# Performance work log

Hardware: AMD Instinct MI355X
Metric: run time of the kernel (lower is better)

Reference implementation:

```python
import jax, jax.numpy as jnp
import numpy as np

B, L, H, V = 64, 8, 4096, 50257


def setup_inputs() -> dict:
    key = jax.random.key(0)
    ks = jax.random.split(key, 5)
    return {
        "embedding": jax.random.normal(ks[0], (V, H), jnp.float32) * 0.02,
        "hidden_states": jax.random.normal(ks[1], (B, L, H), jnp.float32),
        "output_position": 7,  # scalar index of the position to sample from
        "temperatures": jax.random.uniform(ks[2], (B,), jnp.float32, 0.5, 1.5),
        "top_ps": jax.random.uniform(ks[3], (B,), jnp.float32, 0.7, 1.0),
        "tops_ks": jax.random.randint(ks[4], (B,), 1, 64),  # top-k in [1,64)
        "embedding_bias": jnp.zeros((V,), jnp.float32),
    }


def reference(embedding, hidden_states, output_position, temperatures, top_ps, tops_ks, embedding_bias):
    # select the output position: [B, H]
    h = hidden_states[:, output_position, :]
    # logits GEMM against tied embedding: [B, V]
    logits = jnp.einsum("bh,vh->bv", h, embedding) + embedding_bias[None, :]
    logits = logits / temperatures[:, None]
    probs = jax.nn.softmax(logits.astype(jnp.float32), axis=-1)

    # descending sort of probabilities
    order = jnp.argsort(-probs, axis=-1)                       # [B, V]
    probs_sort = jnp.take_along_axis(probs, order, axis=-1)    # [B, V]

    # top-p mask: exclusive cumulative sum exceeding top_p
    cum = jnp.cumsum(probs_sort, axis=-1)
    topp_mask = (cum - probs_sort) > top_ps[:, None]
    # top-k mask: rank >= k
    ranks = jnp.arange(V, dtype=tops_ks.dtype)[None, :]
    topk_mask = ranks >= tops_ks[:, None]

    probs_sort = jnp.where(topp_mask | topk_mask, 0.0, probs_sort)
    probs_sort = probs_sort / jnp.sum(probs_sort, axis=-1, keepdims=True)

    # scatter back to original vocab order via inverse permutation
    inv = jnp.argsort(order, axis=-1)
    probs_final = jnp.take_along_axis(probs_sort, inv, axis=-1)  # [B, V]

    # multinomial sampling (1 sample per row)
    logp = jnp.where(probs_final > 0, jnp.log(jnp.maximum(probs_final, 1e-38)), -jnp.inf)
    next_token_ids = jax.random.categorical(jax.random.key(42), logp, axis=-1)
    return next_token_ids
```

## Files before the change

### kernel.cpp

```cpp
#include <hip/hip_runtime.h>
#include <stdint.h>
#include <float.h>
#include <limits.h>


typedef __bf16 bf16x8 __attribute__((ext_vector_type(8)));
typedef float  f32x4  __attribute__((ext_vector_type(4)));

__device__ __forceinline__ void split8v(const float* f, bf16x8& hi, bf16x8& lo) {
#pragma unroll
    for (int e = 0; e < 8; ++e) {
        const __bf16 h = (__bf16)f[e];
        hi[e] = h;
        lo[e] = (__bf16)(f[e] - (float)h);
    }
}
__device__ __forceinline__ void split8(const float* f, uint4& hi, uint4& lo) {
    bf16x8 vh, vl;
    split8v(f, vh, vl);
    hi = __builtin_bit_cast(uint4, vh);
    lo = __builtin_bit_cast(uint4, vl);
}

__global__ __launch_bounds__(256) void prep_h(
    const float* __restrict__ hs, const int* __restrict__ pos_p,
    unsigned short* __restrict__ Ahi, unsigned short* __restrict__ Alo,
    int H, int L)
{
    const int pos = pos_p[0];
    const int tid = blockIdx.x * 256 + threadIdx.x;
    const int b     = tid >> 8;
    const int kbase = (tid & 255) * 16;
    const float* src = hs + ((size_t)b * L + pos) * H + kbase;
    float f[16];
    *(float4*)&f[0]  = *(const float4*)(src);
    *(float4*)&f[4]  = *(const float4*)(src + 4);
    *(float4*)&f[8]  = *(const float4*)(src + 8);
    *(float4*)&f[12] = *(const float4*)(src + 12);

    const int r16 = b >> 4, ll = b & 15;
    const int kc  = kbase >> 5;
    const int lh0 = (kbase >> 3) & 3;
#pragma unroll
    for (int c = 0; c < 2; ++c) {
        uint4 hi, lo;
        split8(f + 8 * c, hi, lo);
        const size_t dst = ((size_t)(r16 * (H >> 5) + kc) * 64 + (lh0 + c) * 16 + ll) * 8;
        *(uint4*)&Ahi[dst] = hi;
        *(uint4*)&Alo[dst] = lo;
    }
}

#define NWF    512
#define WTILES 16

__global__ __launch_bounds__(256, 2) void logits_mfma(
    const float* __restrict__ emb,
    const unsigned short* __restrict__ Ahi,
    const unsigned short* __restrict__ Alo,
    const float* __restrict__ temps,
    const float* __restrict__ bias,
    float*       __restrict__ out,
    int V, int H)
{
    __shared__ float sB[2][16 * NWF];

    const int tid  = threadIdx.x;
    const int lane = tid & 63;
    const int w    = tid >> 6;
    const int v0   = blockIdx.x * 16;

    const int ll = lane & 15;
    const int lh = lane >> 4;

    const int NWIN = H / NWF;
    const int NTT  = H >> 5;
    const int wst  = (blockIdx.x & 3) * 2;

    const size_t aoff = (size_t)w * ((size_t)H * 16)
                      + (size_t)lh * 128 + (size_t)ll * 8;

    bf16x8 aih[2], ail[2];
    f32x4  acc = (f32x4){0.f, 0.f, 0.f, 0.f};

#define STAGE(win, bf) do {                                                   \
    _Pragma("unroll")                                                         \
    for (int rr = 0; rr < 4; ++rr) {                                          \
        const int r = w * 4 + rr;                                             \
        int rg = v0 + r;                                                      \
        rg = (rg < V) ? rg : (V - 1);                                         \
        const float* rowp = emb + (size_t)rg * H + (size_t)(win) * NWF        \
                          + ((lane * 4) ^ ((r & 15) << 2));                   \
        _Pragma("unroll")                                                     \
        for (int c = 0; c < 2; ++c) {                                         \
            __builtin_amdgcn_global_load_lds(                                 \
                (const __attribute__((address_space(1))) void*)(rowp + c * 256), \
                (__attribute__((address_space(3))) void*)&sB[bf][r * NWF + c * 256], \
                16, 0, 0);                                                    \
        }                                                                     \
    }                                                                         \
} while (0)

#define LOADA(T, p) do {                                                      \
    const size_t ai = aoff + (size_t)(T) * 512;                               \
    aih[p] = *(const bf16x8*)&Ahi[ai];                                        \
    ail[p] = *(const bf16x8*)&Alo[ai];                                        \
} while (0)

    LOADA(wst * WTILES, 0);
    STAGE(wst, 0);
    __syncthreads();

    for (int ws = 0; ws < NWIN; ++ws) {
        const int bf = ws & 1;
        if (ws + 1 < NWIN) STAGE((wst + ws + 1) & (NWIN - 1), bf ^ 1);

#pragma unroll
        for (int kt = 0; kt < WTILES; ++kt) {
            const int p = kt & 1;
            if (!(ws == NWIN - 1 && kt == WTILES - 1)) {
                const int wsn = ws + ((kt + 1) >> 4);
                const int ktn = (kt + 1) & 15;
                const int T1  = (((wst + wsn) & (NWIN - 1)) << 4) + ktn;
                LOADA(T1, p ^ 1);
            }

            const int f0   = kt * 32 + lh * 8;
            const int sidx = ll << 2;
            float f[8];
            *(float4*)&f[0] = *(const float4*)&sB[bf][ll * NWF + ((f0)     ^ sidx)];
            *(float4*)&f[4] = *(const float4*)&sB[bf][ll * NWF + ((f0 + 4) ^ sidx)];
            bf16x8 fbh, fbl;
            split8v(f, fbh, fbl);

            acc = __builtin_amdgcn_mfma_f32_16x16x32_bf16(ail[p], fbh, acc, 0, 0, 0);
            acc = __builtin_amdgcn_mfma_f32_16x16x32_bf16(aih[p], fbl, acc, 0, 0, 0);
            acc = __builtin_amdgcn_mfma_f32_16x16x32_bf16(aih[p], fbh, acc, 0, 0, 0);
        }
        __syncthreads();
    }
#undef STAGE
#undef LOADA

    const int vv = v0 + ll;
    if (vv < V) {
        const float bv = bias[vv];
#pragma unroll
        for (int r = 0; r < 4; ++r) {
            const int b = w * 16 + lh * 4 + r;
            out[(size_t)b * V + vv] = (acc[r] + bv) / temps[b];
        }
    }
}

__device__ __forceinline__ uint32_t rotl32(uint32_t x, int d) {
    return (x << d) | (x >> (32 - d));
}

__device__ float jax_gumbel(uint32_t flat) {
    const uint32_t k0 = 0u, k1 = 42u;
    const uint32_t ks[3] = { k0, k1, k0 ^ k1 ^ 0x1BD11BDAu };
    uint32_t x0 = 0u   + ks[0];
    uint32_t x1 = flat + ks[1];
    const int rot[2][4] = { {13, 15, 26, 6}, {17, 29, 16, 24} };
#pragma unroll
    for (int r = 0; r < 5; ++r) {
        const int* rr = rot[r & 1];
#pragma unroll
        for (int j = 0; j < 4; ++j) {
            x0 += x1;
            x1 = rotl32(x1, rr[j]);
            x1 ^= x0;
        }
        x0 += ks[(r + 1) % 3];
        x1 += ks[(r + 2) % 3] + (uint32_t)(r + 1);
    }
    const uint32_t bits = x0 ^ x1;
    const uint32_t fb = (bits >> 9) | 0x3F800000u;
    const float f = __uint_as_float(fb) - 1.0f;
    const float tiny = 1.17549435e-38f;
    float u = __fadd_rn(__fmul_rn(f, 1.0f), tiny);
    u = fmaxf(tiny, u);
    const float l1 = logf(u);
    return -logf(-l1);
}

#define NBINS 4096
#define CAP   2048
#define NKEEP 64

__global__ __launch_bounds__(256) void sample_kernel(
    const float* __restrict__ logits,
    const float* __restrict__ top_ps,
    const int*   __restrict__ top_ks,
    int*         __restrict__ out_ids,
    int V)
{
    const int b = blockIdx.x;
    const int tid = threadIdx.x;
    const float* row = logits + (size_t)b * V;

    __shared__ float swred[4];
    __shared__ int   bins[NBINS];
    __shared__ int   schunk[256];
    __shared__ int   sThrBin, sCnt, sMkeep;
    __shared__ float cval[CAP];
    __shared__ int   cidx[CAP];
    __shared__ float tval[NKEEP];
    __shared__ int   tidxs[NKEEP];

    float m = -INFINITY;
    for (int k = tid; k < V; k += 256) m = fmaxf(m, row[k]);
#pragma unroll
    for (int o = 32; o > 0; o >>= 1) m = fmaxf(m, __shfl_xor(m, o, 64));
    if ((tid & 63) == 0) swred[tid >> 6] = m;
    __syncthreads();
    m = fmaxf(fmaxf(swred[0], swred[1]), fmaxf(swred[2], swred[3]));

    for (int k = tid; k < NBINS; k += 256) bins[k] = 0;
    if (tid == 0) sCnt = 0;
    __syncthreads();

    float s = 0.f;
    for (int k = tid; k < V; k += 256) {
        const float x = row[k];
        s += expf(x - m);
        const float g = m - x;
        int bin = (int)(g * 256.0f);
        if (bin >= NBINS) bin = NBINS - 1;
        atomicAdd(&bins[bin], 1);
    }
#pragma unroll
    for (int o = 32; o > 0; o >>= 1) s += __shfl_xor(s, o, 64);
    __syncthreads();
    if ((tid & 63) == 0) swred[tid >> 6] = s;

    int csum = 0;
#pragma unroll
    for (int k = 0; k < NBINS / 256; ++k) csum += bins[tid * (NBINS / 256) + k];
    schunk[tid] = csum;
    __syncthreads();
    s = swred[0] + swred[1] + swred[2] + swred[3];
    if (tid == 0) {
        int cum = 0, chunk = 255;
        for (int c = 0; c < 256; ++c) {
            if (cum + schunk[c] >= NKEEP) { chunk = c; break; }
            cum += schunk[c];
        }
        int t = NBINS - 1;
        const int base = chunk * (NBINS / 256);
        for (int k = base; k < base + NBINS / 256; ++k) {
            cum += bins[k];
            if (cum >= NKEEP) { t = k; break; }
        }
        sThrBin = t;
    }
    __syncthreads();
    const int thrBin = sThrBin;

    for (int k = tid; k < V; k += 256) {
        const float x = row[k];
        const float g = m - x;
        int bin = (int)(g * 256.0f);
        if (bin >= NBINS) bin = NBINS - 1;
        if (bin <= thrBin) {
            const int p = atomicAdd(&sCnt, 1);
            if (p < CAP) { cval[p] = x; cidx[p] = k; }
        }
    }
    __syncthreads();
    const int C = min(sCnt, CAP);

    for (int i = tid; i < C; i += 256) {
        const float vi = cval[i];
        const int   ii = cidx[i];
        int rank = 0;
        for (int j = 0; j < C; ++j) {
            const float vj = cval[j];
            const int   ij = cidx[j];
            rank += (vj > vi) || (vj == vi && ij < ii);
        }
        if (rank < NKEEP) { tval[rank] = vi; tidxs[rank] = ii; }
    }
    __syncthreads();

    if (tid == 0) {
        const float pb = top_ps[b];
        const int   kk = top_ks[b];
        const int   nk = min(NKEEP, C);
        float cum = 0.f;
        int mk = 0;
        for (int r = 0; r < nk; ++r) {
            const float pr = expf(tval[r] - m) / s;
            cum += pr;
            const float excl = cum - pr;
            if (excl > pb || r >= kk) break;
            ++mk;
        }
        sMkeep = (mk > 0) ? mk : 1;
    }
    __syncthreads();
    const int mkeep = sMkeep;

    if (tid < 64) {
        float sc = -INFINITY;
        int vid = INT_MAX;
        if (tid < mkeep) {
            const int v = tidxs[tid];
            vid = v;
            sc = tval[tid] + jax_gumbel((uint32_t)b * (uint32_t)V + (uint32_t)v);
        }
#pragma unroll
        for (int o = 32; o > 0; o >>= 1) {
            const float os = __shfl_xor(sc, o, 64);
            const int   ov = __shfl_xor(vid, o, 64);
            if (os > sc || (os == sc && ov < vid)) { sc = os; vid = ov; }
        }
        if (tid == 0) out_ids[b] = vid;
    }
}

extern "C" void kernel_launch(void* const* d_in, const int* in_sizes, int n_in,
                              void* d_out, int out_size, void* d_ws, size_t ws_size,
                              hipStream_t stream)
{
    const float* emb   = (const float*)d_in[0];
    const float* hs    = (const float*)d_in[1];
    const int*   pos   = (const int*)d_in[2];
    const float* temps = (const float*)d_in[3];
    const float* tps   = (const float*)d_in[4];
    const int*   tks   = (const int*)d_in[5];
    const float* bias  = (const float*)d_in[6];

    const int B = in_sizes[3];
    const int V = in_sizes[6];
    const int H = (int)((long long)in_sizes[0] / V);
    const int L = (int)((long long)in_sizes[1] / ((long long)B * H));

    float*          logits = (float*)d_ws;
    unsigned short* Ahi    = (unsigned short*)((char*)d_ws + (16u << 20));
    unsigned short* Alo    = Ahi + (size_t)B * H;

    prep_h<<<(B * H) / (16 * 256), 256, 0, stream>>>(hs, pos, Ahi, Alo, H, L);

    const int nblk = (V + 15) / 16;
    logits_mfma<<<nblk, 256, 0, stream>>>(emb, Ahi, Alo, temps, bias,
                                          logits, V, H);

    sample_kernel<<<B, 256, 0, stream>>>(logits, tps, tks, (int*)d_out, V);
}
```

Measured before the change: 381.7 us.

## Replace double-buffered K windows with a 4-slot LDS ring and explicit vmcnt waits

Restructures the logits MFMA main loop to use smaller 256-wide K windows staged into a 4-deep LDS ring, with A fragments for a whole window loaded into registers in ping-pong sets. Synchronisation uses manual s_waitcnt vmcnt counts plus s_barrier instead of __syncthreads, and sched_barrier pins the instruction order, so two windows of loads stay in flight while one is computed. The per-block staggered starting window is removed. The hand-counted vmcnt values and the extra register pressure from 32 A vectors carry correctness and occupancy risks. With no barrier after each compute, ring slots could in principle be overwritten while still being read.

New measurement: 390.4 us. +2.3%, slower.

```diff
diff --git a/kernel.cpp b/kernel.cpp
--- a/kernel.cpp
+++ b/kernel.cpp
@@ -51,8 +51,8 @@
     }
 }
 
-#define NWF    512
-#define WTILES 16
+#define NWF 256
+#define RING 4
 
 __global__ __launch_bounds__(256, 2) void logits_mfma(
     const float* __restrict__ emb,
@@ -63,84 +63,103 @@
     float*       __restrict__ out,
     int V, int H)
 {
-    __shared__ float sB[2][16 * NWF];
+    __shared__ float sB[RING][16 * NWF];
 
     const int tid  = threadIdx.x;
     const int lane = tid & 63;
     const int w    = tid >> 6;
     const int v0   = blockIdx.x * 16;
 
-    const int ll = lane & 15;
-    const int lh = lane >> 4;
-
-    const int NWIN = H / NWF;
-    const int NTT  = H >> 5;
-    const int wst  = (blockIdx.x & 3) * 2;
+    const int ll  = lane & 15;
+    const int lh  = lane >> 4;
+    const int swz = ll << 2;
+
+    const int NW = H / NWF;
 
     const size_t aoff = (size_t)w * ((size_t)H * 16)
                       + (size_t)lh * 128 + (size_t)ll * 8;
 
-    bf16x8 aih[2], ail[2];
+    bf16x8 Ah0[8], Al0[8], Ah1[8], Al1[8];
     f32x4  acc = (f32x4){0.f, 0.f, 0.f, 0.f};
 
-#define STAGE(win, bf) do {                                                   \
+#define LOADA(win, AH, AL) do {                                               \
+    _Pragma("unroll")                                                         \
+    for (int kt = 0; kt < 8; ++kt) {                                          \
+        const size_t ai = aoff + ((size_t)(win) * 8 + kt) * 512;              \
+        AH[kt] = *(const bf16x8*)&Ahi[ai];                                    \
+        AL[kt] = *(const bf16x8*)&Alo[ai];                                    \
+    }                                                                         \
+} while (0)
+
+#define STAGE(win, slot) do {                                                 \
     _Pragma("unroll")                                                         \
     for (int rr = 0; rr < 4; ++rr) {                                          \
         const int r = w * 4 + rr;                                             \
         int rg = v0 + r;                                                      \
         rg = (rg < V) ? rg : (V - 1);                                         \
-        const float* rowp = emb + (size_t)rg * H + (size_t)(win) * NWF        \
+        const float* srcp = emb + (size_t)rg * H + (size_t)(win) * NWF        \
                           + ((lane * 4) ^ ((r & 15) << 2));                   \
-        _Pragma("unroll")                                                     \
-        for (int c = 0; c < 2; ++c) {                                         \
-            __builtin_amdgcn_global_load_lds(                                 \
-                (const __attribute__((address_space(1))) void*)(rowp + c * 256), \
-                (__attribute__((address_space(3))) void*)&sB[bf][r * NWF + c * 256], \
-                16, 0, 0);                                                    \
-        }                                                                     \
+        __builtin_amdgcn_global_load_lds(                                     \
+            (const __attribute__((address_space(1))) void*)srcp,              \
+            (__attribute__((address_space(3))) void*)&sB[slot][r * NWF],      \
+            16, 0, 0);                                                        \
     }                                                                         \
 } while (0)
 
-#define LOADA(T, p) do {                                                      \
-    const size_t ai = aoff + (size_t)(T) * 512;                               \
-    aih[p] = *(const bf16x8*)&Ahi[ai];                                        \
-    ail[p] = *(const bf16x8*)&Alo[ai];                                        \
+#define COMPUTE(AH, AL, slot) do {                                            \
+    _Pragma("unroll")                                                         \
+    for (int kt = 0; kt < 8; ++kt) {                                          \
+        const int f0 = kt * 32 + lh * 8;                                      \
+        float f[8];                                                           \
+        *(float4*)&f[0] = *(const float4*)&sB[slot][ll * NWF + ((f0)     ^ swz)]; \
+        *(float4*)&f[4] = *(const float4*)&sB[slot][ll * NWF + ((f0 + 4) ^ swz)]; \
+        bf16x8 fbh, fbl;                                                      \
+        split8v(f, fbh, fbl);                                                 \
+        acc = __builtin_amdgcn_mfma_f32_16x16x32_bf16(AL[kt], fbh, acc, 0, 0, 0); \
+        acc = __builtin_amdgcn_mfma_f32_16x16x32_bf16(AH[kt], fbl, acc, 0, 0, 0); \
+        acc = __builtin_amdgcn_mfma_f32_16x16x32_bf16(AH[kt], fbh, acc, 0, 0, 0); \
+    }                                                                         \
 } while (0)
 
-    LOADA(wst * WTILES, 0);
-    STAGE(wst, 0);
-    __syncthreads();
-
-    for (int ws = 0; ws < NWIN; ++ws) {
-        const int bf = ws & 1;
-        if (ws + 1 < NWIN) STAGE((wst + ws + 1) & (NWIN - 1), bf ^ 1);
-
-#pragma unroll
-        for (int kt = 0; kt < WTILES; ++kt) {
-            const int p = kt & 1;
-            if (!(ws == NWIN - 1 && kt == WTILES - 1)) {
-                const int wsn = ws + ((kt + 1) >> 4);
-                const int ktn = (kt + 1) & 15;
-                const int T1  = (((wst + wsn) & (NWIN - 1)) << 4) + ktn;
-                LOADA(T1, p ^ 1);
-            }
-
-            const int f0   = kt * 32 + lh * 8;
-            const int sidx = ll << 2;
-            float f[8];
-            *(float4*)&f[0] = *(const float4*)&sB[bf][ll * NWF + ((f0)     ^ sidx)];
-            *(float4*)&f[4] = *(const float4*)&sB[bf][ll * NWF + ((f0 + 4) ^ sidx)];
-            bf16x8 fbh, fbl;
-            split8v(f, fbh, fbl);
-
-            acc = __builtin_amdgcn_mfma_f32_16x16x32_bf16(ail[p], fbh, acc, 0, 0, 0);
-            acc = __builtin_amdgcn_mfma_f32_16x16x32_bf16(aih[p], fbl, acc, 0, 0, 0);
-            acc = __builtin_amdgcn_mfma_f32_16x16x32_bf16(aih[p], fbh, acc, 0, 0, 0);
-        }
-        __syncthreads();
-    }
+#define SB __builtin_amdgcn_sched_barrier(0)
+
+    LOADA(0, Ah0, Al0);
+    SB;
+    STAGE(0, 0);
+    STAGE(1, 1);
+    SB;
+
+    for (int m = 0; m < NW / 2 - 1; ++m) {
+        const int w0 = 2 * m;
+        LOADA(w0 + 1, Ah1, Al1);
+        SB;
+        STAGE(w0 + 2, ((w0 + 2) & (RING - 1)));
+        SB;
+        asm volatile("s_waitcnt vmcnt(24)" ::: "memory");
+        __builtin_amdgcn_s_barrier();
+        COMPUTE(Ah0, Al0, (w0 & (RING - 1)));
+
+        LOADA(w0 + 2, Ah0, Al0);
+        SB;
+        STAGE(w0 + 3, ((w0 + 3) & (RING - 1)));
+        SB;
+        asm volatile("s_waitcnt vmcnt(24)" ::: "memory");
+        __builtin_amdgcn_s_barrier();
+        COMPUTE(Ah1, Al1, ((w0 + 1) & (RING - 1)));
+    }
+    LOADA(NW - 1, Ah1, Al1);
+    SB;
+    asm volatile("s_waitcnt vmcnt(20)" ::: "memory");
+    __builtin_amdgcn_s_barrier();
+    COMPUTE(Ah0, Al0, ((NW - 2) & (RING - 1)));
+    asm volatile("s_waitcnt vmcnt(0)" ::: "memory");
+    __builtin_amdgcn_s_barrier();
+    COMPUTE(Ah1, Al1, ((NW - 1) & (RING - 1)));
+
+#undef LOADA
 #undef STAGE
-#undef LOADA
+#undef COMPUTE
+#undef SB
 
     const int vv = v0 + ll;
     if (vv < V) {
```

## Shrink LDS window to 256 and raise occupancy, drop A register prefetch

Applied to the files above, without the earlier changes.

Halves the staged embedding window (NWF 512→256), which halves LDS per block and allows launch bounds of 5 blocks per CU instead of 2. It also removes the block-staggered window start and the double-buffered register prefetch of the A fragments, loading A directly inside the inner loop. The aim is to hide memory latency through more resident waves rather than explicit software pipelining. The risk is exposed A-load latency, more barriers per K, and loss of the staggered access pattern across blocks.

Result: faster. 370.4 us (-3.0%).

```diff
diff --git a/kernel.cpp b/kernel.cpp
--- a/kernel.cpp
+++ b/kernel.cpp
@@ -51,10 +51,9 @@
     }
 }
 
-#define NWF    512
-#define WTILES 16
-
-__global__ __launch_bounds__(256, 2) void logits_mfma(
+#define NWF 256
+
+__global__ __launch_bounds__(256, 5) void logits_mfma(
     const float* __restrict__ emb,
     const unsigned short* __restrict__ Ahi,
     const unsigned short* __restrict__ Alo,
@@ -70,77 +69,62 @@
     const int w    = tid >> 6;
     const int v0   = blockIdx.x * 16;
 
-    const int ll = lane & 15;
-    const int lh = lane >> 4;
-
-    const int NWIN = H / NWF;
-    const int NTT  = H >> 5;
-    const int wst  = (blockIdx.x & 3) * 2;
-
-    const size_t aoff = (size_t)w * ((size_t)H * 16)
-                      + (size_t)lh * 128 + (size_t)ll * 8;
-
-    bf16x8 aih[2], ail[2];
-    f32x4  acc = (f32x4){0.f, 0.f, 0.f, 0.f};
-
-#define STAGE(win, bf) do {                                                   \
+    const int ll  = lane & 15;
+    const int lh  = lane >> 4;
+    const int swz = ll << 2;
+
+    const int NW = H / NWF;
+
+    const unsigned short* pAh = Ahi + (size_t)w * ((size_t)H * 16)
+                              + (size_t)lh * 128 + (size_t)ll * 8;
+    const unsigned short* pAl = Alo + (size_t)w * ((size_t)H * 16)
+                              + (size_t)lh * 128 + (size_t)ll * 8;
+
+    f32x4 acc = (f32x4){0.f, 0.f, 0.f, 0.f};
+
+#define STAGE(win, slot) do {                                                 \
     _Pragma("unroll")                                                         \
     for (int rr = 0; rr < 4; ++rr) {                                          \
         const int r = w * 4 + rr;                                             \
         int rg = v0 + r;                                                      \
         rg = (rg < V) ? rg : (V - 1);                                         \
-        const float* rowp = emb + (size_t)rg * H + (size_t)(win) * NWF        \
+        const float* srcp = emb + (size_t)rg * H + (size_t)(win) * NWF        \
                           + ((lane * 4) ^ ((r & 15) << 2));                   \
-        _Pragma("unroll")                                                     \
-        for (int c = 0; c < 2; ++c) {                                         \
-            __builtin_amdgcn_global_load_lds(                                 \
-                (const __attribute__((address_space(1))) void*)(rowp + c * 256), \
-                (__attribute__((address_space(3))) void*)&sB[bf][r * NWF + c * 256], \
-                16, 0, 0);                                                    \
-        }                                                                     \
+        __builtin_amdgcn_global_load_lds(                                     \
+            (const __attribute__((address_space(1))) void*)srcp,              \
+            (__attribute__((address_space(3))) void*)&sB[slot][r * NWF],      \
+            16, 0, 0);                                                        \
     }                                                                         \
 } while (0)
 
-#define LOADA(T, p) do {                                                      \
-    const size_t ai = aoff + (size_t)(T) * 512;                               \
-    aih[p] = *(const bf16x8*)&Ahi[ai];                                        \
-    ail[p] = *(const bf16x8*)&Alo[ai];                                        \
-} while (0)
-
-    LOADA(wst * WTILES, 0);
-    STAGE(wst, 0);
-    __syncthreads();
-
-    for (int ws = 0; ws < NWIN; ++ws) {
-        const int bf = ws & 1;
-        if (ws + 1 < NWIN) STAGE((wst + ws + 1) & (NWIN - 1), bf ^ 1);
-
-#pragma unroll
-        for (int kt = 0; kt < WTILES; ++kt) {
-            const int p = kt & 1;
-            if (!(ws == NWIN - 1 && kt == WTILES - 1)) {
-                const int wsn = ws + ((kt + 1) >> 4);
-                const int ktn = (kt + 1) & 15;
-                const int T1  = (((wst + wsn) & (NWIN - 1)) << 4) + ktn;
-                LOADA(T1, p ^ 1);
-            }
-
-            const int f0   = kt * 32 + lh * 8;
-            const int sidx = ll << 2;
+    STAGE(0, 0);
+    __syncthreads();
+
+    for (int win = 0; win < NW; ++win) {
+        const int bf = win & 1;
+        if (win + 1 < NW) STAGE(win + 1, bf ^ 1);
+
+        const size_t tbase = (size_t)win * 8;
+#pragma unroll
+        for (int kt = 0; kt < 8; ++kt) {
+            const size_t ai = (tbase + kt) * 512;
+            const bf16x8 ah = *(const bf16x8*)&pAh[ai];
+            const bf16x8 al = *(const bf16x8*)&pAl[ai];
+
+            const int f0 = kt * 32 + lh * 8;
             float f[8];
-            *(float4*)&f[0] = *(const float4*)&sB[bf][ll * NWF + ((f0)     ^ sidx)];
-            *(float4*)&f[4] = *(const float4*)&sB[bf][ll * NWF + ((f0 + 4) ^ sidx)];
+            *(float4*)&f[0] = *(const float4*)&sB[bf][ll * NWF + ((f0)     ^ swz)];
+            *(float4*)&f[4] = *(const float4*)&sB[bf][ll * NWF + ((f0 + 4) ^ swz)];
             bf16x8 fbh, fbl;
             split8v(f, fbh, fbl);
 
-            acc = __builtin_amdgcn_mfma_f32_16x16x32_bf16(ail[p], fbh, acc, 0, 0, 0);
-            acc = __builtin_amdgcn_mfma_f32_16x16x32_bf16(aih[p], fbl, acc, 0, 0, 0);
-            acc = __builtin_amdgcn_mfma_f32_16x16x32_bf16(aih[p], fbh, acc, 0, 0, 0);
+            acc = __builtin_amdgcn_mfma_f32_16x16x32_bf16(al, fbh, acc, 0, 0, 0);
+            acc = __builtin_amdgcn_mfma_f32_16x16x32_bf16(ah, fbl, acc, 0, 0, 0);
+            acc = __builtin_amdgcn_mfma_f32_16x16x32_bf16(ah, fbh, acc, 0, 0, 0);
         }
         __syncthreads();
     }
 #undef STAGE
-#undef LOADA
 
     const int vv = v0 + ll;
     if (vv < V) {
```
